# Kernel tuning notes

Measured on AMD Instinct MI355X. Metric: run time of the kernel, lower is better.

Reference implementation:

```python
import jax, jax.numpy as jnp
from jax import lax
import numpy as np

# Layer configs from mnist_classifier_conv2d.__init__:
# (in_ch, out_ch, kernel, stride)
_LAYERS = [(1, 16, 2, 2), (16, 16, 2, 2), (16, 16, 2, 1), (16, 16, 2, 2), (16, 16, 2, 2), (16, 10, 1, 1)]


def _binarize(x):
    # (x > 0).float() * 2 - 1  ->  +1 / -1
    return jnp.where(x > 0, jnp.float32(1.0), jnp.float32(-1.0))


def _nand_conv(x, w, stride):
    # Conv2d_Nand: binarize weights to +/-1, convolve (AND-style accumulation
    # over the +/-1 domain), then negate-and-threshold (NAND) back to +/-1.
    wb = _binarize(w)  # [O, I, kH, kW]
    y = lax.conv_general_dilated(
        x, wb,
        window_strides=(stride, stride),
        padding='VALID',
        dimension_numbers=('NCHW', 'OIHW', 'NCHW'))
    # NAND = NOT(AND): positive activation -> -1, else +1
    return jnp.where(y > 0, jnp.float32(-1.0), jnp.float32(1.0))


def setup_inputs() -> dict:
    key = jax.random.key(0)
    keys = jax.random.split(key, 7)
    B = 32768
    inp = {'x': jax.random.normal(keys[0], (B, 1, 28, 28), dtype=jnp.float32)}
    for i, (ci, co, k, s) in enumerate(_LAYERS):
        inp[f'w{i}'] = jax.random.normal(keys[i + 1], (co, ci, k, k), dtype=jnp.float32)
    return inp


def reference(x, w0, w1, w2, w3, w4, w5):
    ws = (w0, w1, w2, w3, w4, w5)
    h = _binarize(x)  # input binarization: (x > 0) * 2 - 1
    for (ci, co, k, s), w in zip(_LAYERS, ws):
        h = _nand_conv(h, w, s)
    # spatial dims collapse to 1x1 -> flatten(1) gives [B, 10]
    return h.reshape(h.shape[0], -1)
```

## Files before the change

kernel.cpp:

```cpp
#include <hip/hip_runtime.h>
#include <stdint.h>

typedef unsigned int u32;
typedef unsigned long long u64;

#define NSAMP 32768

__device__ __forceinline__ u32 bfe4(u32 v, int off) { return (v >> off) & 15u; }

__global__ __launch_bounds__(256, 4) void nand_net_kernel(
        const float* __restrict__ x,
        const float* __restrict__ w0, const float* __restrict__ w1,
        const float* __restrict__ w2, const float* __restrict__ w3,
        const float* __restrict__ w4, const float* __restrict__ w5,
        float* __restrict__ out) {

    __shared__ u32 lut[256];
    __shared__ u32 Wl[4][16][2];
    __shared__ u32 W5m[10];
    __shared__ u64 pkLDS[4][8][12];

    const int tid  = threadIdx.x;
    const int lane = tid & 63;
    const int w    = tid >> 6;

    {
        u32 nib[16];
        #pragma unroll
        for (int oc = 0; oc < 16; ++oc) {
            float4 f = ((const float4*)w0)[oc];
            nib[oc] = (f.x > 0.f ? 1u : 0u) | (f.y > 0.f ? 2u : 0u) |
                      (f.z > 0.f ? 4u : 0u) | (f.w > 0.f ? 8u : 0u);
        }
        {
            int e = tid;
            u32 na = e & 15u, nb = (u32)e >> 4;
            u32 idxA = (na & 3u) | ((nb & 3u) << 2);
            u32 idxB = (na >> 2) | ((nb >> 2) << 2);
            u32 cvA = 0, cvB = 0;
            #pragma unroll
            for (int oc = 0; oc < 16; ++oc) {
                cvA |= (__popc(idxA ^ nib[oc]) >= 2 ? 1u : 0u) << oc;
                cvB |= (__popc(idxB ^ nib[oc]) >= 2 ? 1u : 0u) << oc;
            }
            lut[e] = cvA | (cvB << 16);
        }
        if (tid < 64) {
            const int L = tid >> 4, oc = tid & 15;
            const float* wp = (L == 0) ? w1 : (L == 1) ? w2 : (L == 2) ? w3 : w4;
            wp += oc * 64;
            float4 g[16];
            #pragma unroll
            for (int i = 0; i < 16; ++i) g[i] = ((const float4*)wp)[i];
            u32 lo = 0, hi = 0;
            #pragma unroll
            for (int ci = 0; ci < 16; ++ci) {
                lo |= (g[ci].x > 0.f ? 1u : 0u) << ci;
                lo |= (g[ci].y > 0.f ? 1u : 0u) << (16 + ci);
                hi |= (g[ci].z > 0.f ? 1u : 0u) << ci;
                hi |= (g[ci].w > 0.f ? 1u : 0u) << (16 + ci);
            }
            Wl[L][oc][0] = lo; Wl[L][oc][1] = hi;
        }
        if (tid < 10) {
            const float* wp = w5 + tid * 16;
            float4 h0 = ((const float4*)wp)[0], h1 = ((const float4*)wp)[1];
            float4 h2 = ((const float4*)wp)[2], h3 = ((const float4*)wp)[3];
            u32 m = 0;
            m |= (h0.x>0.f?1u:0u)      | (h0.y>0.f?2u:0u)      | (h0.z>0.f?4u:0u)      | (h0.w>0.f?8u:0u);
            m |= (h1.x>0.f?16u:0u)     | (h1.y>0.f?32u:0u)     | (h1.z>0.f?64u:0u)     | (h1.w>0.f?128u:0u);
            m |= (h2.x>0.f?256u:0u)    | (h2.y>0.f?512u:0u)    | (h2.z>0.f?1024u:0u)   | (h2.w>0.f?2048u:0u);
            m |= (h3.x>0.f?4096u:0u)   | (h3.y>0.f?8192u:0u)   | (h3.z>0.f?16384u:0u)  | (h3.w>0.f?32768u:0u);
            W5m[tid] = m;
        }
    }

    const int sbase = blockIdx.x * 32 + w * 8;
    {
        const int rhalf = lane >> 5;
        const int col   = lane & 31;
        const float* xw = x + (size_t)sbase * 784 + rhalf * 28 + col;

        float va[2][10], vb[2][10];
        #define LOADB(buf, sb)                                          \
            _Pragma("unroll")                                           \
            for (int j = 0; j < 2; ++j) {                               \
                const float* xs = xw + (size_t)((sb) + j) * 784;        \
                _Pragma("unroll")                                       \
                for (int k = 0; k < 10; ++k) buf[j][k] = xs[k * 56];    \
            }
        #define PROCB(buf, sb)                                          \
            _Pragma("unroll")                                           \
            for (int j = 0; j < 2; ++j) {                               \
                u64 word = 0;                                           \
                _Pragma("unroll")                                       \
                for (int k = 0; k < 10; ++k) {                          \
                    u64 m = __ballot(buf[j][k] > 0.0f);                 \
                    if (lane == k) word = m;                            \
                }                                                       \
                if (lane < 10) pkLDS[w][(sb) + j][lane] = word;         \
            }

        LOADB(va, 0)
        LOADB(vb, 2)
        PROCB(va, 0) LOADB(va, 4)
        PROCB(vb, 2) LOADB(vb, 6)
        PROCB(va, 4)
        PROCB(vb, 6)
        #undef LOADB
        #undef PROCB
    }
    __syncthreads();

    const int s8  = lane >> 3;
    const int q   = lane & 7;
    const int ocb = q * 2;
    const int s   = sbase + s8;

    u32 r[20];
    {
        const uint4* qa = (const uint4*)(&pkLDS[w][s8][0]);
        #pragma unroll
        for (int i = 0; i < 5; ++i) {
            uint4 v = qa[i];
            r[4*i] = v.x; r[4*i+1] = v.y; r[4*i+2] = v.z; r[4*i+3] = v.w;
        }
    }

    u32 wlo[2], whi[2];
    #define LOADW(L)                                                   \
        _Pragma("unroll")                                              \
        for (int j = 0; j < 2; ++j) {                                  \
            wlo[j] = Wl[L][ocb + j][0]; whi[j] = Wl[L][ocb + j][1];    \
        }

    #define CONV16(dst, LO, HI)                                        \
        {                                                              \
            u32 _lo = (LO), _hi = (HI), _my = 0;                       \
            _Pragma("unroll")                                          \
            for (int j = 0; j < 2; ++j) {                              \
                u32 _m = __popc(_lo ^ wlo[j]) + __popc(_hi ^ whi[j]) + 32u; \
                _my |= ((_m >> 6) & 1u) << (ocb + j);                  \
            }                                                          \
            _my |= (u32)__shfl_xor((int)_my, 1, 64);                   \
            _my |= (u32)__shfl_xor((int)_my, 2, 64);                   \
            dst = _my | (u32)__shfl_xor((int)_my, 4, 64);              \
        }

    u32 cv1[5][5];
    LOADW(0)
    #pragma unroll
    for (int Y = 0; Y < 5; ++Y) {
        #pragma unroll
        for (int X = 0; X < 5; ++X) {
            u32 eA = bfe4(r[4*Y],     4*X) | (bfe4(r[4*Y + 1], 4*X) << 4);
            u32 eB = bfe4(r[4*Y + 2], 4*X) | (bfe4(r[4*Y + 3], 4*X) << 4);
            CONV16(cv1[Y][X], lut[eA], lut[eB])
        }
    }

    u32 cv2[4][4];
    LOADW(1)
    #pragma unroll
    for (int y = 0; y < 4; ++y) {
        #pragma unroll
        for (int x = 0; x < 4; ++x) {
            CONV16(cv2[y][x],
                   cv1[y][x]     | (cv1[y][x+1]     << 16),
                   cv1[y+1][x]   | (cv1[y+1][x+1]   << 16))
        }
    }

    u32 cv3[2][2];
    LOADW(2)
    #pragma unroll
    for (int y = 0; y < 2; ++y) {
        #pragma unroll
        for (int x = 0; x < 2; ++x) {
            CONV16(cv3[y][x],
                   cv2[2*y][2*x]   | (cv2[2*y][2*x+1]   << 16),
                   cv2[2*y+1][2*x] | (cv2[2*y+1][2*x+1] << 16))
        }
    }

    u32 cv4;
    LOADW(3)
    CONV16(cv4,
           cv3[0][0] | (cv3[0][1] << 16),
           cv3[1][0] | (cv3[1][1] << 16))

    float* o = out + (size_t)s * 10;
    {
        u32 m = __popc(cv4 ^ W5m[q]);
        o[q] = (m <= 7u) ? -1.0f : 1.0f;
        if (q < 2) {
            u32 m2 = __popc(cv4 ^ W5m[q + 8]);
            o[q + 8] = (m2 <= 7u) ? -1.0f : 1.0f;
        }
    }
    #undef CONV16
    #undef LOADW
}

extern "C" void kernel_launch(void* const* d_in, const int* in_sizes, int n_in,
                              void* d_out, int out_size, void* d_ws, size_t ws_size,
                              hipStream_t stream) {
    const float* x  = (const float*)d_in[0];
    const float* w0 = (const float*)d_in[1];
    const float* w1 = (const float*)d_in[2];
    const float* w2 = (const float*)d_in[3];
    const float* w3 = (const float*)d_in[4];
    const float* w4 = (const float*)d_in[5];
    const float* w5 = (const float*)d_in[6];

    nand_net_kernel<<<1024, 256, 0, stream>>>(x, w0, w1, w2, w3, w4, w5,
                                              (float*)d_out);
}
```

Before: 160.6 us.

## Split input bit-packing into a separate kernel staging packed words in workspace

Moves the input load-and-ballot packing stage into its own kernel that writes packed bit words to global workspace, and makes the network kernel read them from global memory instead of LDS. It also adds scheduling barriers to keep loads ahead of the ballot work. The aim is to separate the memory-bound phase from the compute phase so each can run at its own occupancy. The cost is an extra launch and a global write and read of the packed data.

```diff
diff --git a/kernel.cpp b/kernel.cpp
--- a/kernel.cpp
+++ b/kernel.cpp
@@ -6,23 +6,66 @@
 
 #define NSAMP 32768
 
+
+__global__ __launch_bounds__(256, 4) void pack_k(const float* __restrict__ x,
+                                                 u64* __restrict__ pk) {
+    const int lane  = threadIdx.x & 63;
+    const int wid   = (blockIdx.x * 256 + threadIdx.x) >> 6;
+    const int sbase = wid * 8;
+    const int rhalf = lane >> 5;
+    const int col   = lane & 31;
+    const float* xw = x + (size_t)sbase * 784 + rhalf * 28 + col;
+
+    float va[2][10], vb[2][10];
+    #define LOADB(buf, sb)                                          \
+        _Pragma("unroll")                                           \
+        for (int j = 0; j < 2; ++j) {                               \
+            const float* xs = xw + (size_t)((sb) + j) * 784;        \
+            _Pragma("unroll")                                       \
+            for (int k = 0; k < 10; ++k) buf[j][k] = xs[k * 56];    \
+        }
+    #define PROCB(buf, sb)                                          \
+        _Pragma("unroll")                                           \
+        for (int j = 0; j < 2; ++j) {                               \
+            u64 word = 0;                                           \
+            _Pragma("unroll")                                       \
+            for (int k = 0; k < 10; ++k) {                          \
+                u64 m = __ballot(buf[j][k] > 0.0f);                 \
+                if (lane == k) word = m;                            \
+            }                                                       \
+            if (lane < 10)                                          \
+                pk[(size_t)(sbase + (sb) + j) * 12 + lane] = word;  \
+        }
+    #define SB __builtin_amdgcn_sched_barrier(0);
+
+    LOADB(va, 0)
+    LOADB(vb, 2)
+    SB
+    PROCB(va, 0) LOADB(va, 4)
+    SB
+    PROCB(vb, 2) LOADB(vb, 6)
+    SB
+    PROCB(va, 4)
+    PROCB(vb, 6)
+    #undef LOADB
+    #undef PROCB
+    #undef SB
+}
+
 __device__ __forceinline__ u32 bfe4(u32 v, int off) { return (v >> off) & 15u; }
 
-__global__ __launch_bounds__(256, 4) void nand_net_kernel(
-        const float* __restrict__ x,
+__global__ __launch_bounds__(256, 4) void net_k(
         const float* __restrict__ w0, const float* __restrict__ w1,
         const float* __restrict__ w2, const float* __restrict__ w3,
         const float* __restrict__ w4, const float* __restrict__ w5,
-        float* __restrict__ out) {
+        const u64* __restrict__ pk, float* __restrict__ out) {
 
     __shared__ u32 lut[256];
     __shared__ u32 Wl[4][16][2];
     __shared__ u32 W5m[10];
-    __shared__ u64 pkLDS[4][8][12];
 
     const int tid  = threadIdx.x;
     const int lane = tid & 63;
-    const int w    = tid >> 6;
 
     {
         u32 nib[16];
@@ -74,52 +117,16 @@
             W5m[tid] = m;
         }
     }
-
-    const int sbase = blockIdx.x * 32 + w * 8;
-    {
-        const int rhalf = lane >> 5;
-        const int col   = lane & 31;
-        const float* xw = x + (size_t)sbase * 784 + rhalf * 28 + col;
-
-        float va[2][10], vb[2][10];
-        #define LOADB(buf, sb)                                          \
-            _Pragma("unroll")                                           \
-            for (int j = 0; j < 2; ++j) {                               \
-                const float* xs = xw + (size_t)((sb) + j) * 784;        \
-                _Pragma("unroll")                                       \
-                for (int k = 0; k < 10; ++k) buf[j][k] = xs[k * 56];    \
-            }
-        #define PROCB(buf, sb)                                          \
-            _Pragma("unroll")                                           \
-            for (int j = 0; j < 2; ++j) {                               \
-                u64 word = 0;                                           \
-                _Pragma("unroll")                                       \
-                for (int k = 0; k < 10; ++k) {                          \
-                    u64 m = __ballot(buf[j][k] > 0.0f);                 \
-                    if (lane == k) word = m;                            \
-                }                                                       \
-                if (lane < 10) pkLDS[w][(sb) + j][lane] = word;         \
-            }
-
-        LOADB(va, 0)
-        LOADB(vb, 2)
-        PROCB(va, 0) LOADB(va, 4)
-        PROCB(vb, 2) LOADB(vb, 6)
-        PROCB(va, 4)
-        PROCB(vb, 6)
-        #undef LOADB
-        #undef PROCB
-    }
     __syncthreads();
 
-    const int s8  = lane >> 3;
-    const int q   = lane & 7;
-    const int ocb = q * 2;
-    const int s   = sbase + s8;
+    const int gwave = (blockIdx.x * 256 + tid) >> 6;
+    const int s     = gwave * 8 + (lane >> 3);
+    const int q     = lane & 7;
+    const int ocb   = q * 2;
 
     u32 r[20];
     {
-        const uint4* qa = (const uint4*)(&pkLDS[w][s8][0]);
+        const uint4* qa = (const uint4*)(pk + (size_t)s * 12);
         #pragma unroll
         for (int i = 0; i < 5; ++i) {
             uint4 v = qa[i];
@@ -212,7 +219,8 @@
     const float* w3 = (const float*)d_in[4];
     const float* w4 = (const float*)d_in[5];
     const float* w5 = (const float*)d_in[6];
-
-    nand_net_kernel<<<1024, 256, 0, stream>>>(x, w0, w1, w2, w3, w4, w5,
-                                              (float*)d_out);
+    u64* pk = (u64*)d_ws;
+
+    pack_k<<<1024, 256, 0, stream>>>(x, pk);
+    net_k<<<1024, 256, 0, stream>>>(w0, w1, w2, w3, w4, w5, pk, (float*)d_out);
 }
```

After: 170.9 us. +6.4%, slower.
